# Optimization experiments

Measured on AMD Instinct MI355X. Metric: run time of the kernel, lower is better.

Reference implementation:

```python
import jax, jax.numpy as jnp
import numpy as np

D_MODEL = 768
NUM_HEADS = 12
HEAD_DIM = D_MODEL // NUM_HEADS


def _trunc_normal(key, shape, std):
    # truncated normal in [-3std, 3std], matching torch.nn.init.trunc_normal_
    return jax.random.truncated_normal(key, -3.0, 3.0, shape, dtype=jnp.float32) * std


def setup_inputs() -> dict:
    key = jax.random.key(0)
    kx, kq, kk, kv, ko = jax.random.split(key, 5)
    std = np.sqrt(2.0 / (D_MODEL + D_MODEL))
    x = jax.random.normal(kx, (4, 2048, D_MODEL), dtype=jnp.float32)
    Wq = _trunc_normal(kq, (D_MODEL, D_MODEL), std)
    Wk = _trunc_normal(kk, (D_MODEL, D_MODEL), std)
    Wv = _trunc_normal(kv, (D_MODEL, D_MODEL), std)
    Wo = _trunc_normal(ko, (D_MODEL, D_MODEL), std)
    return {"x": x, "Wq": Wq, "Wk": Wk, "Wv": Wv, "Wo": Wo}


def reference(x, Wq, Wk, Wv, Wo):
    b, s, _ = x.shape
    h, d = NUM_HEADS, HEAD_DIM
    # Linear: einsum 'b s i, o i -> b s o'
    Q = jnp.einsum('bsi,oi->bso', x, Wq).reshape(b, s, h, d).transpose(0, 2, 1, 3)
    K = jnp.einsum('bsi,oi->bso', x, Wk).reshape(b, s, h, d).transpose(0, 2, 1, 3)
    V = jnp.einsum('bsi,oi->bso', x, Wv).reshape(b, s, h, d).transpose(0, 2, 1, 3)
    scores = jnp.einsum('bhqd,bhkd->bhqk', Q, K) / jnp.sqrt(jnp.float32(d))
    causal = jnp.tril(jnp.ones((s, s), dtype=bool))  # (s, s)
    scores = jnp.where(causal, scores, jnp.float32(-jnp.inf))
    attn = jax.nn.softmax(scores, axis=-1)
    out = jnp.einsum('bhqk,bhkd->bhqd', attn, V)  # (b, h, s, d)
    out = out.transpose(0, 2, 1, 3).reshape(b, s, h * d)
    return jnp.einsum('bsi,oi->bso', out, Wo)
```

## Files before the change

kernel.cpp:

```cpp
#include <hip/hip_runtime.h>
#include <hip/hip_bf16.h>

#define SEQ   2048
#define BATCH 4
#define DM    768
#define NH    12
#define HD    64
#define MTOT  (BATCH*SEQ)

typedef short bf16x8 __attribute__((ext_vector_type(8)));
typedef float f32x4  __attribute__((ext_vector_type(4)));

static __device__ __forceinline__ short f2bf(float f) {
  union { __hip_bfloat16 h; short s; } u;
  u.h = __float2bfloat16(f);
  return u.s;
}

static __device__ __forceinline__ void async_cp16(const short* g, short* l) {
  __builtin_amdgcn_global_load_lds(
      (const __attribute__((address_space(1))) void*)g,
      (__attribute__((address_space(3))) void*)l, 16, 0, 0);
}

__global__ void cvt5_kernel(const float* __restrict__ x, const float* __restrict__ wq,
                            const float* __restrict__ wk, const float* __restrict__ wv,
                            const float* __restrict__ wo, short* __restrict__ dst) {
  const int NX4 = MTOT * DM / 4, NW4 = DM * DM / 4, TOT4 = NX4 + 4 * NW4;
  int i = blockIdx.x * blockDim.x + threadIdx.x;
  if (i >= TOT4) return;
  const float* src; int off;
  if (i < NX4) { src = x; off = i; }
  else {
    int j = i - NX4; int sel = j / NW4; off = j - sel * NW4;
    src = (sel == 0) ? wq : (sel == 1) ? wk : (sel == 2) ? wv : wo;
  }
  float4 v = reinterpret_cast<const float4*>(src)[off];
  short4 o;
  o.x = f2bf(v.x); o.y = f2bf(v.y); o.z = f2bf(v.z); o.w = f2bf(v.w);
  reinterpret_cast<short4*>(dst)[i] = o;
}

static __device__ __forceinline__ void gemm_lds_core(
    const short* __restrict__ A, const short* __restrict__ W,
    short* As, short* Bs, int m0, int n0, f32x4 acc[4][4])
{
  const int t = threadIdx.x;
  const int lane = t & 63, w = t >> 6;
  const int quad = lane >> 4, lq = lane & 15;
  const int mw = (w & 1) * 64, nw = (w >> 1) * 64;
  const int r0 = t >> 2, c0 = (t & 3) * 8;
  const short* ga0 = A + (size_t)(m0 + r0) * DM + c0;
  const short* ga1 = A + (size_t)(m0 + 64 + r0) * DM + c0;
  const short* gb0 = W + (size_t)(n0 + r0) * DM + c0;
  const short* gb1 = W + (size_t)(n0 + 64 + r0) * DM + c0;
  short* la0 = As + t * 8;
  short* la1 = As + 2048 + t * 8;
  short* lb0 = Bs + t * 8;
  short* lb1 = Bs + 2048 + t * 8;

  for (int k0 = 0; k0 < DM; k0 += 32) {
    async_cp16(ga0 + k0, la0);
    async_cp16(ga1 + k0, la1);
    async_cp16(gb0 + k0, lb0);
    async_cp16(gb1 + k0, lb1);
    __syncthreads();
    bf16x8 af[4], bf[4];
#pragma unroll
    for (int i = 0; i < 4; ++i) {
      af[i] = *(const bf16x8*)(As + (mw + i * 16 + lq) * 32 + quad * 8);
      bf[i] = *(const bf16x8*)(Bs + (nw + i * 16 + lq) * 32 + quad * 8);
    }
#pragma unroll
    for (int mt = 0; mt < 4; ++mt)
#pragma unroll
      for (int nt = 0; nt < 4; ++nt)
        acc[mt][nt] = __builtin_amdgcn_mfma_f32_16x16x32_bf16(af[mt], bf[nt], acc[mt][nt], 0, 0, 0);
    __syncthreads();
  }
}

__global__ __launch_bounds__(256) void qkv_gemm(
    const short* __restrict__ xb, const short* __restrict__ Wall,
    short* __restrict__ Qb, short* __restrict__ Kb, short* __restrict__ VTb)
{
  __shared__ __align__(16) short As[4096], Bs[4096];
  const int m0 = blockIdx.y * 128, n0 = blockIdx.x * 128;
  f32x4 acc[4][4] = {};
  gemm_lds_core(xb, Wall, As, Bs, m0, n0, acc);

  const int t = threadIdx.x;
  const int lane = t & 63, w = t >> 6;
  const int quad = lane >> 4, lq = lane & 15;
  const int mwb = m0 + (w & 1) * 64, nwb = n0 + (w >> 1) * 64;
#pragma unroll
  for (int mt = 0; mt < 4; ++mt)
#pragma unroll
    for (int nt = 0; nt < 4; ++nt) {
      const int n = nwb + nt * 16 + lq;
      const int z = n / DM, nn = n % DM;
      const int h = nn >> 6, d = nn & 63;
      const int mbase = mwb + mt * 16 + quad * 4;
      const int b = mbase >> 11, s0 = mbase & 2047;
      if (z == 2) {
        short4 v;
        v.x = f2bf(acc[mt][nt][0]); v.y = f2bf(acc[mt][nt][1]);
        v.z = f2bf(acc[mt][nt][2]); v.w = f2bf(acc[mt][nt][3]);
        *(short4*)(VTb + ((size_t)(b * NH + h) * HD + d) * SEQ + s0) = v;
      } else {
        short* dst = (z == 0) ? Qb : Kb;
#pragma unroll
        for (int r = 0; r < 4; ++r)
          dst[((size_t)(b * NH + h) * SEQ + s0 + r) * HD + d] = f2bf(acc[mt][nt][r]);
      }
    }
}

__global__ __launch_bounds__(256) void attn_kernel(
    const short* __restrict__ Qb, const short* __restrict__ Kb,
    const short* __restrict__ VTb, short* __restrict__ AOb)
{
  __shared__ __align__(16) short Ks[32 * 64];
  __shared__ __align__(16) short Vs[64 * 32];
  const int bp = blockIdx.x;
  const int bh = bp % 48;
  const int g  = bp / 48;
  const int tid = threadIdx.x;
  const int w = tid >> 6, lane = tid & 63;
  const int quad = lane >> 4, lq = lane & 15;
  const int tp = 4 * g + w;
  const int b = bh / NH, h = bh % NH;
  const int q0b = 16 * tp;
  const int q1b = 2032 - 16 * tp;
  const int E0 = q0b + 16;
  const int E1 = q1b + 16;
  const int Eblk = 2048 - 64 * g;

  const short* Qh = Qb  + (size_t)bh * SEQ * HD;
  const short* Kh = Kb  + (size_t)bh * SEQ * HD;
  const short* Vh = VTb + (size_t)bh * HD * SEQ;

  bf16x8 qf0[2], qf1[2];
#pragma unroll
  for (int hh = 0; hh < 2; ++hh) {
    qf0[hh] = *(const bf16x8*)(Qh + (size_t)(q0b + lq) * HD + hh * 32 + quad * 8);
    qf1[hh] = *(const bf16x8*)(Qh + (size_t)(q1b + lq) * HD + hh * 32 + quad * 8);
  }

  f32x4 o0[4] = {}, o1[4] = {};
  float m0v = -3e38f, m1v = -3e38f;
  float l0v = 0.0f, l1v = 0.0f;
  const float Cc = 0.18033688011112042f;

  const int srow = tid >> 3, sslot = tid & 7;
  const int sswz = (srow & 3) | (((srow >> 3) & 1) << 2);
  const short* gK = Kh + (size_t)srow * HD + (sslot ^ sswz) * 8;
  const short* gV = Vh + (size_t)(tid >> 2) * SEQ + (tid & 3) * 8;
  short* lK = Ks + tid * 8;
  short* lV = Vs + tid * 8;

  const int rswz = (lq & 3) | (((lq >> 2) & 1) << 2);

  for (int kb = 0; kb < Eblk; kb += 32) {
    async_cp16(gK + (size_t)kb * HD, lK);
    async_cp16(gV + kb, lV);
    __syncthreads();
    if (kb < E1) {
      const bool act0 = kb < E0;
      f32x4 st0[2] = {}, st1[2] = {};
#pragma unroll
      for (int t2 = 0; t2 < 2; ++t2) {
        const int row = 8 * (lq >> 2) + 4 * t2 + (lq & 3);
        const int sl0 = quad ^ rswz;
        bf16x8 k0 = *(const bf16x8*)(Ks + row * 64 + sl0 * 8);
        bf16x8 k1 = *(const bf16x8*)(Ks + row * 64 + (sl0 ^ 4) * 8);
        st1[t2] = __builtin_amdgcn_mfma_f32_16x16x32_bf16(k0, qf1[0], st1[t2], 0, 0, 0);
        st1[t2] = __builtin_amdgcn_mfma_f32_16x16x32_bf16(k1, qf1[1], st1[t2], 0, 0, 0);
        if (act0) {
          st0[t2] = __builtin_amdgcn_mfma_f32_16x16x32_bf16(k0, qf0[0], st0[t2], 0, 0, 0);
          st0[t2] = __builtin_amdgcn_mfma_f32_16x16x32_bf16(k1, qf0[1], st0[t2], 0, 0, 0);
        }
      }
      bf16x8 vf[4];
#pragma unroll
      for (int mt = 0; mt < 4; ++mt)
        vf[mt] = *(const bf16x8*)(Vs + (mt * 16 + lq) * 32 + quad * 8);

      bf16x8 pf1;
      {
        const int qv = q1b + lq;
        float mx = -3e38f;
#pragma unroll
        for (int t2 = 0; t2 < 2; ++t2)
#pragma unroll
          for (int r = 0; r < 4; ++r) {
            const int key = kb + 8 * quad + 4 * t2 + r;
            const float v = (key <= qv) ? st1[t2][r] : -3e38f;
            st1[t2][r] = v;
            mx = fmaxf(mx, v);
          }
        mx = fmaxf(mx, __shfl_xor(mx, 16));
        mx = fmaxf(mx, __shfl_xor(mx, 32));
        const float mn = fmaxf(m1v, mx);
        const float al = __builtin_amdgcn_exp2f((m1v - mn) * Cc);
        m1v = mn;
        float rs = 0.0f;
#pragma unroll
        for (int t2 = 0; t2 < 2; ++t2)
#pragma unroll
          for (int r = 0; r < 4; ++r) {
            const float p = __builtin_amdgcn_exp2f((st1[t2][r] - mn) * Cc);
            rs += p;
            pf1[t2 * 4 + r] = f2bf(p);
          }
        rs += __shfl_xor(rs, 16);
        rs += __shfl_xor(rs, 32);
        if (!__all(al == 1.0f)) {
          l1v *= al;
#pragma unroll
          for (int mt = 0; mt < 4; ++mt)
#pragma unroll
            for (int r = 0; r < 4; ++r)
              o1[mt][r] *= al;
        }
        l1v += rs;
      }
      bf16x8 pf0;
      if (act0) {
        const int qv = q0b + lq;
        float mx = -3e38f;
#pragma unroll
        for (int t2 = 0; t2 < 2; ++t2)
#pragma unroll
          for (int r = 0; r < 4; ++r) {
            const int key = kb + 8 * quad + 4 * t2 + r;
            const float v = (key <= qv) ? st0[t2][r] : -3e38f;
            st0[t2][r] = v;
            mx = fmaxf(mx, v);
          }
        mx = fmaxf(mx, __shfl_xor(mx, 16));
        mx = fmaxf(mx, __shfl_xor(mx, 32));
        const float mn = fmaxf(m0v, mx);
        const float al = __builtin_amdgcn_exp2f((m0v - mn) * Cc);
        m0v = mn;
        float rs = 0.0f;
#pragma unroll
        for (int t2 = 0; t2 < 2; ++t2)
#pragma unroll
          for (int r = 0; r < 4; ++r) {
            const float p = __builtin_amdgcn_exp2f((st0[t2][r] - mn) * Cc);
            rs += p;
            pf0[t2 * 4 + r] = f2bf(p);
          }
        rs += __shfl_xor(rs, 16);
        rs += __shfl_xor(rs, 32);
        if (!__all(al == 1.0f)) {
          l0v *= al;
#pragma unroll
          for (int mt = 0; mt < 4; ++mt)
#pragma unroll
            for (int r = 0; r < 4; ++r)
              o0[mt][r] *= al;
        }
        l0v += rs;
      }
#pragma unroll
      for (int mt = 0; mt < 4; ++mt) {
        o1[mt] = __builtin_amdgcn_mfma_f32_16x16x32_bf16(vf[mt], pf1, o1[mt], 0, 0, 0);
        if (act0)
          o0[mt] = __builtin_amdgcn_mfma_f32_16x16x32_bf16(vf[mt], pf0, o0[mt], 0, 0, 0);
      }
    }
    __syncthreads();
  }

  {
    const float inv = 1.0f / l1v;
    const int q = q1b + lq;
#pragma unroll
    for (int mt = 0; mt < 4; ++mt) {
      short4 v;
      v.x = f2bf(o1[mt][0] * inv);
      v.y = f2bf(o1[mt][1] * inv);
      v.z = f2bf(o1[mt][2] * inv);
      v.w = f2bf(o1[mt][3] * inv);
      *(short4*)(AOb + ((size_t)(b * SEQ + q)) * DM + h * HD + mt * 16 + quad * 4) = v;
    }
  }
  {
    const float inv = 1.0f / l0v;
    const int q = q0b + lq;
#pragma unroll
    for (int mt = 0; mt < 4; ++mt) {
      short4 v;
      v.x = f2bf(o0[mt][0] * inv);
      v.y = f2bf(o0[mt][1] * inv);
      v.z = f2bf(o0[mt][2] * inv);
      v.w = f2bf(o0[mt][3] * inv);
      *(short4*)(AOb + ((size_t)(b * SEQ + q)) * DM + h * HD + mt * 16 + quad * 4) = v;
    }
  }
}

__global__ __launch_bounds__(256) void out_gemm(
    const short* __restrict__ AOb, const short* __restrict__ Wob, float* __restrict__ C)
{
  __shared__ __align__(16) short As[4096], Bs[4096];
  const int m0 = blockIdx.y * 128, n0 = blockIdx.x * 128;
  f32x4 acc[4][4] = {};
  gemm_lds_core(AOb, Wob, As, Bs, m0, n0, acc);

  const int t = threadIdx.x;
  const int lane = t & 63, w = t >> 6;
  const int quad = lane >> 4, lq = lane & 15;
  const int mwb = m0 + (w & 1) * 64, nwb = n0 + (w >> 1) * 64;
#pragma unroll
  for (int mt = 0; mt < 4; ++mt)
#pragma unroll
    for (int nt = 0; nt < 4; ++nt) {
      const int n = nwb + nt * 16 + lq;
      const int mbase = mwb + mt * 16 + quad * 4;
#pragma unroll
      for (int r = 0; r < 4; ++r)
        C[(size_t)(mbase + r) * DM + n] = acc[mt][nt][r];
    }
}

extern "C" void kernel_launch(void* const* d_in, const int* in_sizes, int n_in,
                              void* d_out, int out_size, void* d_ws, size_t ws_size,
                              hipStream_t stream) {
  const float* x  = (const float*)d_in[0];
  const float* Wq = (const float*)d_in[1];
  const float* Wk = (const float*)d_in[2];
  const float* Wv = (const float*)d_in[3];
  const float* Wo = (const float*)d_in[4];
  float* out = (float*)d_out;

  short* xb  = (short*)d_ws;
  short* Wqb = xb  + (size_t)MTOT * DM;
  short* Wkb = Wqb + DM * DM;
  short* Wvb = Wkb + DM * DM;
  short* Wob = Wvb + DM * DM;
  short* Qb  = Wob + DM * DM;
  short* Kb  = Qb  + (size_t)MTOT * DM;
  short* VTb = Kb  + (size_t)MTOT * DM;
  short* AOb = xb;

  const int TOT4 = (MTOT * DM + 4 * DM * DM) / 4;
  cvt5_kernel<<<(TOT4 + 255) / 256, 256, 0, stream>>>(x, Wq, Wk, Wv, Wo, xb);

  qkv_gemm<<<dim3(3 * DM / 128, MTOT / 128), 256, 0, stream>>>(xb, Wqb, Qb, Kb, VTb);
  attn_kernel<<<dim3(768), 256, 0, stream>>>(Qb, Kb, VTb, AOb);
  out_gemm<<<dim3(DM / 128, MTOT / 128), 256, 0, stream>>>(AOb, Wob, out);
}
```

Measured before the change: 237.1 us.

## Compute softmax row sums via MFMA with ones, pack bf16 pairs, remap blocks

Row sums of the softmax probabilities are now produced by an extra MFMA that multiplies a vector of bf16 ones by the probability fragment, replacing the per-lane adds and two cross-lane shuffles. The exponent uses a single fmaf with a precomputed scaled max, and the bf16 conversion packs pairs with __float22bfloat162_rn. The block index mapping changes so consecutive blocks share a head instead of sharing a query group. The sums now accumulate the bf16-rounded probabilities, which matches what multiplies V but differs slightly from the fp32 sums used before.

```diff
diff --git a/kernel.cpp b/kernel.cpp
--- a/kernel.cpp
+++ b/kernel.cpp
@@ -123,8 +123,8 @@
   __shared__ __align__(16) short Ks[32 * 64];
   __shared__ __align__(16) short Vs[64 * 32];
   const int bp = blockIdx.x;
-  const int bh = bp % 48;
-  const int g  = bp / 48;
+  const int bh = bp >> 4;
+  const int g  = bp & 15;
   const int tid = threadIdx.x;
   const int w = tid >> 6, lane = tid & 63;
   const int quad = lane >> 4, lq = lane & 15;
@@ -147,9 +147,13 @@
     qf1[hh] = *(const bf16x8*)(Qh + (size_t)(q1b + lq) * HD + hh * 32 + quad * 8);
   }
 
+  bf16x8 onesf;
+#pragma unroll
+  for (int j = 0; j < 8; ++j) onesf[j] = (short)0x3F80;
+
   f32x4 o0[4] = {}, o1[4] = {};
+  f32x4 lacc0 = {}, lacc1 = {};
   float m0v = -3e38f, m1v = -3e38f;
-  float l0v = 0.0f, l1v = 0.0f;
   const float Cc = 0.18033688011112042f;
 
   const int srow = tid >> 3, sslot = tid & 7;
@@ -204,26 +208,27 @@
         const float mn = fmaxf(m1v, mx);
         const float al = __builtin_amdgcn_exp2f((m1v - mn) * Cc);
         m1v = mn;
-        float rs = 0.0f;
-#pragma unroll
-        for (int t2 = 0; t2 < 2; ++t2)
-#pragma unroll
-          for (int r = 0; r < 4; ++r) {
-            const float p = __builtin_amdgcn_exp2f((st1[t2][r] - mn) * Cc);
-            rs += p;
-            pf1[t2 * 4 + r] = f2bf(p);
-          }
-        rs += __shfl_xor(rs, 16);
-        rs += __shfl_xor(rs, 32);
         if (!__all(al == 1.0f)) {
-          l1v *= al;
+#pragma unroll
+          for (int r = 0; r < 4; ++r) lacc1[r] *= al;
 #pragma unroll
           for (int mt = 0; mt < 4; ++mt)
 #pragma unroll
             for (int r = 0; r < 4; ++r)
               o1[mt][r] *= al;
         }
-        l1v += rs;
+        const float mC = mn * Cc;
+        float p[8];
+#pragma unroll
+        for (int t2 = 0; t2 < 2; ++t2)
+#pragma unroll
+          for (int r = 0; r < 4; ++r)
+            p[t2 * 4 + r] = __builtin_amdgcn_exp2f(fmaf(st1[t2][r], Cc, -mC));
+        union { bf16x8 v; __hip_bfloat162 h[4]; } u;
+#pragma unroll
+        for (int j = 0; j < 4; ++j)
+          u.h[j] = __float22bfloat162_rn(make_float2(p[2 * j], p[2 * j + 1]));
+        pf1 = u.v;
       }
       bf16x8 pf0;
       if (act0) {
@@ -243,26 +248,27 @@
         const float mn = fmaxf(m0v, mx);
         const float al = __builtin_amdgcn_exp2f((m0v - mn) * Cc);
         m0v = mn;
-        float rs = 0.0f;
-#pragma unroll
-        for (int t2 = 0; t2 < 2; ++t2)
-#pragma unroll
-          for (int r = 0; r < 4; ++r) {
-            const float p = __builtin_amdgcn_exp2f((st0[t2][r] - mn) * Cc);
-            rs += p;
-            pf0[t2 * 4 + r] = f2bf(p);
-          }
-        rs += __shfl_xor(rs, 16);
-        rs += __shfl_xor(rs, 32);
         if (!__all(al == 1.0f)) {
-          l0v *= al;
+#pragma unroll
+          for (int r = 0; r < 4; ++r) lacc0[r] *= al;
 #pragma unroll
           for (int mt = 0; mt < 4; ++mt)
 #pragma unroll
             for (int r = 0; r < 4; ++r)
               o0[mt][r] *= al;
         }
-        l0v += rs;
+        const float mC = mn * Cc;
+        float p[8];
+#pragma unroll
+        for (int t2 = 0; t2 < 2; ++t2)
+#pragma unroll
+          for (int r = 0; r < 4; ++r)
+            p[t2 * 4 + r] = __builtin_amdgcn_exp2f(fmaf(st0[t2][r], Cc, -mC));
+        union { bf16x8 v; __hip_bfloat162 h[4]; } u;
+#pragma unroll
+        for (int j = 0; j < 4; ++j)
+          u.h[j] = __float22bfloat162_rn(make_float2(p[2 * j], p[2 * j + 1]));
+        pf0 = u.v;
       }
 #pragma unroll
       for (int mt = 0; mt < 4; ++mt) {
@@ -270,12 +276,15 @@
         if (act0)
           o0[mt] = __builtin_amdgcn_mfma_f32_16x16x32_bf16(vf[mt], pf0, o0[mt], 0, 0, 0);
       }
+      lacc1 = __builtin_amdgcn_mfma_f32_16x16x32_bf16(onesf, pf1, lacc1, 0, 0, 0);
+      if (act0)
+        lacc0 = __builtin_amdgcn_mfma_f32_16x16x32_bf16(onesf, pf0, lacc0, 0, 0, 0);
     }
     __syncthreads();
   }
 
   {
-    const float inv = 1.0f / l1v;
+    const float inv = 1.0f / lacc1[0];
     const int q = q1b + lq;
 #pragma unroll
     for (int mt = 0; mt < 4; ++mt) {
@@ -288,7 +297,7 @@
     }
   }
   {
-    const float inv = 1.0f / l0v;
+    const float inv = 1.0f / lacc0[0];
     const int q = q0b + lq;
 #pragma unroll
     for (int mt = 0; mt < 4; ++mt) {
```

Measured after the change: 239.7 us. About the same (+1.1%).
